# Performance work log

Hardware: AMD Instinct MI355X
Metric: run time of the kernel (lower is better)

## Reference

```python
import jax, jax.numpy as jnp
import numpy as np

B, N, M, D, H, K, V = 2, 2048, 2048, 1024, 16, 64, 64
MAX_WAVELENGTH = 10000
SCALE_FACTOR = 1.0


def rope(x, positions, max_wavelength, scale_factor):
    # x: [b, s, h, k]; positions: [b, s] int
    head_dim = x.shape[-1]
    fraction = 2.0 * jnp.arange(head_dim // 2, dtype=x.dtype) / head_dim
    timescale = jnp.asarray(max_wavelength, x.dtype) ** fraction            # [k/2]
    # scaled positions -> phase per (b, s, 1 head bcast, k/2)
    phase = (positions.astype(x.dtype) / scale_factor)[:, :, None, None] / timescale  # [b,s,1,k/2]
    sin, cos = jnp.sin(phase), jnp.cos(phase)
    x1, x2 = jnp.split(x, 2, axis=-1)
    return jnp.concatenate([x1 * cos - x2 * sin, x2 * cos + x1 * sin], axis=-1)


def setup_inputs() -> dict:
    key = jax.random.key(0)
    ks = jax.random.split(key, 8)
    scale = 1.0 / np.sqrt(D)  # keep logits numerically sane with random params
    inp = {
        "query": jax.random.normal(ks[0], (B, N, D), jnp.float32),
        "q_positions": jnp.broadcast_to(jnp.arange(N, dtype=jnp.int32), (B, N)),
        "key": jax.random.normal(ks[1], (B, M, D), jnp.float32),
        "k_positions": jnp.broadcast_to(jnp.arange(M, dtype=jnp.int32), (B, M)),
        "value": jax.random.normal(ks[2], (B, M, D), jnp.float32),
        "mask": jnp.ones((1, 1, N, M), dtype=bool),
        "P_q": jax.random.normal(ks[3], (H, D, K), jnp.float32) * scale,
        "P_k": jax.random.normal(ks[4], (H, D, K), jnp.float32) * scale,
        "P_v": jax.random.normal(ks[5], (H, D, V), jnp.float32) * scale,
        "P_o": jax.random.normal(ks[6], (H, D, V), jnp.float32) * scale,
    }
    return inp


def reference(query, q_positions, key, k_positions, value, mask, P_q, P_k, P_v, P_o):
    q = jnp.einsum('bnd,hdk->bnhk', query, P_q)
    k = jnp.einsum('bmd,hdk->bmhk', key, P_k)
    v = jnp.einsum('bmd,hdv->bmhv', value, P_v)
    q = rope(q, q_positions, MAX_WAVELENGTH, SCALE_FACTOR)
    k = rope(k, k_positions, MAX_WAVELENGTH, SCALE_FACTOR)
    logits = jnp.einsum('bnhk,bmhk->bhnm', q, k)
    if mask is not None:
        logits = jnp.where(mask, logits, -jnp.inf)
    weights = jax.nn.softmax(logits, axis=-1)
    o = jnp.einsum('bhnm,bmhv->bnhv', weights, v)
    return jnp.einsum('bnhv,hdv->bnd', o, P_o)
```

## Files before the change

kernel.cpp:

```cpp
#include <hip/hip_runtime.h>
#include <hip/hip_bf16.h>
#include <math.h>

#define B_ 2
#define N_ 2048
#define M_ 2048
#define D_ 1024
#define H_ 16


typedef _Float16 f16;
typedef f16  f16x4 __attribute__((ext_vector_type(4)));
typedef f16  f16x8 __attribute__((ext_vector_type(8)));
typedef float f32x4  __attribute__((ext_vector_type(4)));
typedef float f32x16 __attribute__((ext_vector_type(16)));

#define MFMA16(a, b, c) __builtin_amdgcn_mfma_f32_16x16x32_f16((a), (b), (c), 0, 0, 0)
#define MFMA32(a, b, c) __builtin_amdgcn_mfma_f32_32x32x16_f16((a), (b), (c), 0, 0, 0)
#define LDST 72

__global__ __launch_bounds__(256) void prep_pt(
    const float* __restrict__ P, f16* __restrict__ Pt)
{
  __shared__ float Ts[64][65];
  const int tid = threadIdx.x;
  const int d0 = blockIdx.x * 64, h = blockIdx.y;
  #pragma unroll
  for (int it = 0; it < 4; ++it) {
    int fi = tid + 256 * it;
    int dr = fi >> 4, c4 = (fi & 15) << 2;
    float4 v = *(const float4*)(P + ((size_t)h * D_ + d0 + dr) * 64 + c4);
    Ts[dr][c4+0] = v.x; Ts[dr][c4+1] = v.y; Ts[dr][c4+2] = v.z; Ts[dr][c4+3] = v.w;
  }
  __syncthreads();
  const int c = tid >> 2, dp = (tid & 3) * 16;
  f16x8 w0, w1;
  #pragma unroll
  for (int i = 0; i < 8; ++i) { w0[i] = (f16)Ts[dp + i][c]; w1[i] = (f16)Ts[dp + 8 + i][c]; }
  f16* dst = Pt + ((size_t)h * 64 + c) * D_ + d0 + dp;
  *(f16x8*)dst = w0;
  *(f16x8*)(dst + 8) = w1;
}

__global__ __launch_bounds__(256) void prep_wo(
    const float* __restrict__ Po, f16* __restrict__ Wo)
{
  int e = (blockIdx.x * 256 + threadIdx.x) * 4;
  if (e >= H_ * D_ * 64) return;
  int h = e >> 16, d = (e >> 6) & 1023, v = e & 63;
  float4 x = *(const float4*)(Po + e);
  f16x4 w = {(f16)x.x, (f16)x.y, (f16)x.z, (f16)x.w};
  *(f16x4*)&Wo[(size_t)d * 1024 + h * 64 + v] = w;
}

__global__ __launch_bounds__(256, 3) void gemm_fused(
    const float* __restrict__ Aq, const float* __restrict__ Ak,
    const float* __restrict__ Av,
    const f16* __restrict__ Bq, const f16* __restrict__ Bk,
    const f16* __restrict__ Bv,
    const int* __restrict__ qpos, const int* __restrict__ kpos,
    f16* __restrict__ dq, f16* __restrict__ dk, f16* __restrict__ dv)
{
  __shared__ f16 As[128 * LDST];
  __shared__ f16 Bs[128 * LDST];
  const int tid = threadIdx.x, lane = tid & 63, wave = tid >> 6;
  const int quad = lane >> 4, l16 = lane & 15;
  const int col0 = blockIdx.x * 128, row0 = blockIdx.y * 128;
  const int op = blockIdx.z;
  const int wr = (wave >> 1) * 64, wc = (wave & 1) * 64;

  const float* A  = (op == 0) ? Aq : (op == 1) ? Ak : Av;
  const f16*  Bt  = (op == 0) ? Bq : (op == 1) ? Bk : Bv;

  f32x4 acc[4][4] = {};

  for (int k0 = 0; k0 < 1024; k0 += 64) {
    #pragma unroll
    for (int it = 0; it < 8; ++it) {
      int fi = tid + 256 * it;
      int row = fi >> 4, c4 = (fi & 15) << 2;
      float4 xv = *(const float4*)(A + (size_t)(row0 + row) * 1024 + k0 + c4);
      f16x4 hv = {(f16)xv.x, (f16)xv.y, (f16)xv.z, (f16)xv.w};
      *(f16x4*)&As[row * LDST + c4] = hv;
    }
    #pragma unroll
    for (int it = 0; it < 4; ++it) {
      int fi = tid + 256 * it;
      int row = fi >> 3, c8 = (fi & 7) * 8;
      *(f16x8*)&Bs[row * LDST + c8] =
          *(const f16x8*)(Bt + (size_t)(col0 + row) * 1024 + k0 + c8);
    }
    __syncthreads();
    #pragma unroll
    for (int ks = 0; ks < 2; ++ks) {
      f16x8 af[4], bf[4];
      #pragma unroll
      for (int i = 0; i < 4; ++i)
        af[i] = *(const f16x8*)&As[(wr + i * 16 + l16) * LDST + ks * 32 + quad * 8];
      #pragma unroll
      for (int j = 0; j < 4; ++j)
        bf[j] = *(const f16x8*)&Bs[(wc + j * 16 + l16) * LDST + ks * 32 + quad * 8];
      #pragma unroll
      for (int i = 0; i < 4; ++i)
        #pragma unroll
        for (int j = 0; j < 4; ++j)
          acc[i][j] = MFMA16(af[i], bf[j], acc[i][j]);
    }
    __syncthreads();
  }

  if (op == 2) {
    #pragma unroll
    for (int i = 0; i < 4; ++i) {
      int r = row0 + wr + i * 16 + quad * 4;
      int b = r >> 11, s = r & 2047;
      #pragma unroll
      for (int j = 0; j < 4; ++j) {
        int col = col0 + wc + j * 16 + l16;
        int h = col >> 6, v = col & 63;
        f16x4 w = {(f16)acc[i][j][0], (f16)acc[i][j][1],
                   (f16)acc[i][j][2], (f16)acc[i][j][3]};
        *(f16x4*)&dv[((size_t)(b * H_ + h) * 64 + v) * 2048 + s] = w;
      }
    }
  } else {
    const int* pos = (op == 0) ? qpos : kpos;
    f16* oq = (op == 0) ? dq : dk;
    #pragma unroll
    for (int i = 0; i < 4; ++i) {
      #pragma unroll
      for (int reg = 0; reg < 4; ++reg) {
        int r = row0 + wr + i * 16 + quad * 4 + reg;
        int b = r >> 11, s = r & 2047;
        float fpos = (float)pos[r];
        #pragma unroll
        for (int j = 0; j < 2; ++j) {
          int col = col0 + wc + j * 16 + l16;
          int h = col >> 6, c = col & 63;
          float inv_ts = exp2f(-(float)c * 0.4152410118609203f);
          float ph = fpos * inv_ts, sn, cs;
          sincosf(ph, &sn, &cs);
          float x1 = acc[i][j][reg], x2 = acc[i][j + 2][reg];
          size_t base = ((size_t)(b * H_ + h) * 2048 + s) * 64;
          oq[base + c]      = (f16)(x1 * cs - x2 * sn);
          oq[base + c + 32] = (f16)(x2 * cs + x1 * sn);
        }
      }
    }
  }
}

__global__ __launch_bounds__(256) void flash4(
    const f16* __restrict__ q, const f16* __restrict__ k,
    const f16* __restrict__ vt, f16* __restrict__ o)
{
  __shared__ f16 Ks[64 * LDST];
  __shared__ f16 Vts[64 * LDST];
  __shared__ f16 Ps[4][32 * LDST];

  const int tid = threadIdx.x, lane = tid & 63, wave = tid >> 6;
  const int L = lane >> 5, nl = lane & 31;
  const int n0 = blockIdx.x * 128;
  const int h = blockIdx.y, b = blockIdx.z;

  const f16* qb = q  + (size_t)(b * H_ + h) * N_ * 64;
  const f16* kb = k  + (size_t)(b * H_ + h) * M_ * 64;
  const f16* vb = vt + (size_t)(b * H_ + h) * 64 * M_;

  f16x8 qf[4];
  #pragma unroll
  for (int g = 0; g < 4; ++g)
    qf[g] = *(const f16x8*)(qb + (size_t)(n0 + wave * 32 + nl) * 64 + g * 16 + L * 8);

  f32x16 acc[2] = {};
  float mst = -INFINITY;
  float lst = 0.f;
  const float L2E = 1.4426950408889634f;

  const int srow = tid >> 2, soff = (tid & 3) * 16;
  f16* psw = Ps[wave];

  for (int m0 = 0; m0 < M_; m0 += 64) {
    *(f16x8*)&Ks[srow * LDST + soff]      = *(const f16x8*)(kb + (size_t)(m0 + srow) * 64 + soff);
    *(f16x8*)&Ks[srow * LDST + soff + 8]  = *(const f16x8*)(kb + (size_t)(m0 + srow) * 64 + soff + 8);
    *(f16x8*)&Vts[srow * LDST + soff]     = *(const f16x8*)(vb + (size_t)srow * M_ + m0 + soff);
    *(f16x8*)&Vts[srow * LDST + soff + 8] = *(const f16x8*)(vb + (size_t)srow * M_ + m0 + soff + 8);
    __syncthreads();

    f32x16 s[2] = {};
    #pragma unroll
    for (int u = 0; u < 2; ++u)
      #pragma unroll
      for (int g = 0; g < 4; ++g) {
        f16x8 af = *(const f16x8*)&Ks[(u * 32 + nl) * LDST + g * 16 + L * 8];
        s[u] = MFMA32(af, qf[g], s[u]);
      }

    float mx = s[0][0];
    #pragma unroll
    for (int u = 0; u < 2; ++u)
      #pragma unroll
      for (int r = 0; r < 16; ++r) mx = fmaxf(mx, s[u][r]);
    mx = fmaxf(mx, __shfl_xor(mx, 32));
    float m_new = fmaxf(mst, mx * L2E);
    float alpha = exp2f(mst - m_new);
    mst = m_new;

    float sum = 0.f;
    float p[2][16];
    #pragma unroll
    for (int u = 0; u < 2; ++u)
      #pragma unroll
      for (int r = 0; r < 16; ++r) {
        float pv = exp2f(s[u][r] * L2E - m_new);
        p[u][r] = pv;
        sum += pv;
      }
    sum += __shfl_xor(sum, 32);
    lst = lst * alpha + sum;

    #pragma unroll
    for (int u = 0; u < 2; ++u)
      #pragma unroll
      for (int rq = 0; rq < 4; ++rq) {
        f16x4 w = {(f16)p[u][rq * 4 + 0], (f16)p[u][rq * 4 + 1],
                   (f16)p[u][rq * 4 + 2], (f16)p[u][rq * 4 + 3]};
        *(f16x4*)&psw[nl * LDST + u * 32 + 8 * rq + 4 * L] = w;
      }
    f16x8 pb[4];
    #pragma unroll
    for (int g = 0; g < 4; ++g)
      pb[g] = *(const f16x8*)&psw[nl * LDST + g * 16 + L * 8];

    #pragma unroll
    for (int u = 0; u < 2; ++u)
      #pragma unroll
      for (int r = 0; r < 16; ++r) acc[u][r] *= alpha;
    #pragma unroll
    for (int u = 0; u < 2; ++u)
      #pragma unroll
      for (int g = 0; g < 4; ++g) {
        f16x8 vf = *(const f16x8*)&Vts[(u * 32 + nl) * LDST + g * 16 + L * 8];
        acc[u] = MFMA32(vf, pb[g], acc[u]);
      }
    __syncthreads();
  }

  float invl = 1.0f / lst;
  f16* ob = o + ((size_t)(b * N_ + n0 + wave * 32 + nl) * 1024) + h * 64;
  #pragma unroll
  for (int u = 0; u < 2; ++u)
    #pragma unroll
    for (int rq = 0; rq < 4; ++rq) {
      f16x4 w = {(f16)(acc[u][rq * 4 + 0] * invl), (f16)(acc[u][rq * 4 + 1] * invl),
                 (f16)(acc[u][rq * 4 + 2] * invl), (f16)(acc[u][rq * 4 + 3] * invl)};
      *(f16x4*)&ob[u * 32 + 8 * rq + 4 * L] = w;
    }
}

__global__ __launch_bounds__(256) void gemm_out(
    const f16* __restrict__ A, const f16* __restrict__ Bt,
    float* __restrict__ out)
{
  __shared__ f16 As[128 * LDST];
  __shared__ f16 Bs[64 * LDST];
  const int tid = threadIdx.x, lane = tid & 63, wave = tid >> 6;
  const int quad = lane >> 4, l16 = lane & 15;
  const int col0 = blockIdx.x * 64, row0 = blockIdx.y * 128;
  const int wr = (wave >> 1) * 64, wc = (wave & 1) * 32;

  f32x4 acc[4][2] = {};

  for (int k0 = 0; k0 < 1024; k0 += 64) {
    #pragma unroll
    for (int it = 0; it < 4; ++it) {
      int fi = tid + 256 * it;
      int row = fi >> 3, c8 = (fi & 7) * 8;
      *(f16x8*)&As[row * LDST + c8] =
          *(const f16x8*)(A + (size_t)(row0 + row) * 1024 + k0 + c8);
    }
    #pragma unroll
    for (int it = 0; it < 2; ++it) {
      int fi = tid + 256 * it;
      int row = fi >> 3, c8 = (fi & 7) * 8;
      *(f16x8*)&Bs[row * LDST + c8] =
          *(const f16x8*)(Bt + (size_t)(col0 + row) * 1024 + k0 + c8);
    }
    __syncthreads();
    #pragma unroll
    for (int ks = 0; ks < 2; ++ks) {
      f16x8 af[4], bf[2];
      #pragma unroll
      for (int i = 0; i < 4; ++i)
        af[i] = *(const f16x8*)&As[(wr + i * 16 + l16) * LDST + ks * 32 + quad * 8];
      #pragma unroll
      for (int j = 0; j < 2; ++j)
        bf[j] = *(const f16x8*)&Bs[(wc + j * 16 + l16) * LDST + ks * 32 + quad * 8];
      #pragma unroll
      for (int i = 0; i < 4; ++i)
        #pragma unroll
        for (int j = 0; j < 2; ++j)
          acc[i][j] = MFMA16(af[i], bf[j], acc[i][j]);
    }
    __syncthreads();
  }

  #pragma unroll
  for (int i = 0; i < 4; ++i)
    #pragma unroll
    for (int j = 0; j < 2; ++j)
      #pragma unroll
      for (int reg = 0; reg < 4; ++reg)
        out[(size_t)(row0 + wr + i * 16 + quad * 4 + reg) * 1024 +
            col0 + wc + j * 16 + l16] = acc[i][j][reg];
}

extern "C" void kernel_launch(void* const* d_in, const int* in_sizes, int n_in,
                              void* d_out, int out_size, void* d_ws, size_t ws_size,
                              hipStream_t stream) {
  (void)in_sizes; (void)n_in; (void)out_size; (void)ws_size;
  const float* query = (const float*)d_in[0];
  const int*   qpos  = (const int*)d_in[1];
  const float* key   = (const float*)d_in[2];
  const int*   kpos  = (const int*)d_in[3];
  const float* value = (const float*)d_in[4];
  const float* Pq = (const float*)d_in[6];
  const float* Pk = (const float*)d_in[7];
  const float* Pv = (const float*)d_in[8];
  const float* Po = (const float*)d_in[9];
  float* out = (float*)d_out;

  const size_t pm = (size_t)1024 * 1024;
  const size_t em = (size_t)B_ * H_ * 2048 * 64;
  f16* Ptq = (f16*)d_ws;
  f16* Ptk = Ptq + pm;
  f16* Ptv = Ptk + pm;
  f16* Wo  = Ptv + pm;
  f16* q_ws  = Wo + pm;
  f16* k_ws  = q_ws + em;
  f16* vt_ws = k_ws + em;
  f16* o_ws  = vt_ws + em;

  dim3 blk(256);
  prep_pt<<<dim3(16, 16), blk, 0, stream>>>(Pq, Ptq);
  prep_pt<<<dim3(16, 16), blk, 0, stream>>>(Pk, Ptk);
  prep_pt<<<dim3(16, 16), blk, 0, stream>>>(Pv, Ptv);
  prep_wo<<<dim3(1024), blk, 0, stream>>>(Po, Wo);

  gemm_fused<<<dim3(8, 32, 3), blk, 0, stream>>>(
      query, key, value, Ptq, Ptk, Ptv, qpos, kpos, q_ws, k_ws, vt_ws);

  flash4<<<dim3(N_ / 128, H_, B_), blk, 0, stream>>>(q_ws, k_ws, vt_ws, o_ws);

  gemm_out<<<dim3(16, 32), blk, 0, stream>>>(o_ws, Wo, out);
}
```

Baseline: 280.0 us.

## Prefetch tiles into registers, merge prep kernels, precompute RoPE tables, skip rescale

```diff
diff --git a/kernel.cpp b/kernel.cpp
--- a/kernel.cpp
+++ b/kernel.cpp
@@ -19,46 +19,62 @@
 #define MFMA32(a, b, c) __builtin_amdgcn_mfma_f32_32x32x16_f16((a), (b), (c), 0, 0, 0)
 #define LDST 72
 
-__global__ __launch_bounds__(256) void prep_pt(
-    const float* __restrict__ P, f16* __restrict__ Pt)
+__global__ __launch_bounds__(256) void prep_all(
+    const float* __restrict__ Pq, const float* __restrict__ Pk,
+    const float* __restrict__ Pv, const float* __restrict__ Po,
+    const int* __restrict__ qpos, const int* __restrict__ kpos,
+    f16* __restrict__ Ptq, f16* __restrict__ Ptk, f16* __restrict__ Ptv,
+    f16* __restrict__ Wo, float2* __restrict__ tabq, float2* __restrict__ tabk)
 {
   __shared__ float Ts[64][65];
-  const int tid = threadIdx.x;
-  const int d0 = blockIdx.x * 64, h = blockIdx.y;
-  #pragma unroll
-  for (int it = 0; it < 4; ++it) {
-    int fi = tid + 256 * it;
-    int dr = fi >> 4, c4 = (fi & 15) << 2;
-    float4 v = *(const float4*)(P + ((size_t)h * D_ + d0 + dr) * 64 + c4);
-    Ts[dr][c4+0] = v.x; Ts[dr][c4+1] = v.y; Ts[dr][c4+2] = v.z; Ts[dr][c4+3] = v.w;
-  }
-  __syncthreads();
-  const int c = tid >> 2, dp = (tid & 3) * 16;
-  f16x8 w0, w1;
-  #pragma unroll
-  for (int i = 0; i < 8; ++i) { w0[i] = (f16)Ts[dp + i][c]; w1[i] = (f16)Ts[dp + 8 + i][c]; }
-  f16* dst = Pt + ((size_t)h * 64 + c) * D_ + d0 + dp;
-  *(f16x8*)dst = w0;
-  *(f16x8*)(dst + 8) = w1;
+  const int z = blockIdx.y, x = blockIdx.x, tid = threadIdx.x;
+  if (z < 3) {
+    if (x >= 256) return;
+    const float* P = (z == 0) ? Pq : (z == 1) ? Pk : Pv;
+    f16* Pt = (z == 0) ? Ptq : (z == 1) ? Ptk : Ptv;
+    const int d0 = (x & 15) * 64, h = x >> 4;
+    #pragma unroll
+    for (int it = 0; it < 4; ++it) {
+      int fi = tid + 256 * it;
+      int dr = fi >> 4, c4 = (fi & 15) << 2;
+      float4 v = *(const float4*)(P + ((size_t)h * D_ + d0 + dr) * 64 + c4);
+      Ts[dr][c4+0] = v.x; Ts[dr][c4+1] = v.y; Ts[dr][c4+2] = v.z; Ts[dr][c4+3] = v.w;
+    }
+    __syncthreads();
+    const int c = tid >> 2, dp = (tid & 3) * 16;
+    f16x8 w0, w1;
+    #pragma unroll
+    for (int i = 0; i < 8; ++i) { w0[i] = (f16)Ts[dp + i][c]; w1[i] = (f16)Ts[dp + 8 + i][c]; }
+    f16* dst = Pt + ((size_t)h * 64 + c) * D_ + d0 + dp;
+    *(f16x8*)dst = w0;
+    *(f16x8*)(dst + 8) = w1;
+  } else if (z == 3) {
+    int e = (x * 256 + tid) * 4;
+    if (e >= H_ * D_ * 64) return;
+    int h = e >> 16, d = (e >> 6) & 1023, v = e & 63;
+    float4 xx = *(const float4*)(Po + e);
+    f16x4 w = {(f16)xx.x, (f16)xx.y, (f16)xx.z, (f16)xx.w};
+    *(f16x4*)&Wo[(size_t)d * 1024 + h * 64 + v] = w;
+  } else {
+    if (x >= 512) return;
+    int idx = x * 256 + tid;
+    int r = idx >> 5, c = idx & 31;
+    const int* pos = (z == 4) ? qpos : kpos;
+    float2* tab = (z == 4) ? tabq : tabk;
+    float fpos = (float)pos[r];
+    float inv_ts = exp2f(-(float)c * 0.4152410118609203f);
+    float ph = fpos * inv_ts, sn, cs;
+    sincosf(ph, &sn, &cs);
+    tab[idx] = make_float2(cs, sn);
+  }
 }
 
-__global__ __launch_bounds__(256) void prep_wo(
-    const float* __restrict__ Po, f16* __restrict__ Wo)
-{
-  int e = (blockIdx.x * 256 + threadIdx.x) * 4;
-  if (e >= H_ * D_ * 64) return;
-  int h = e >> 16, d = (e >> 6) & 1023, v = e & 63;
-  float4 x = *(const float4*)(Po + e);
-  f16x4 w = {(f16)x.x, (f16)x.y, (f16)x.z, (f16)x.w};
-  *(f16x4*)&Wo[(size_t)d * 1024 + h * 64 + v] = w;
-}
-
-__global__ __launch_bounds__(256, 3) void gemm_fused(
+__global__ __launch_bounds__(256) void gemm_fused(
     const float* __restrict__ Aq, const float* __restrict__ Ak,
     const float* __restrict__ Av,
     const f16* __restrict__ Bq, const f16* __restrict__ Bk,
     const f16* __restrict__ Bv,
-    const int* __restrict__ qpos, const int* __restrict__ kpos,
+    const float2* __restrict__ tabq, const float2* __restrict__ tabk,
     f16* __restrict__ dq, f16* __restrict__ dk, f16* __restrict__ dv)
 {
   __shared__ f16 As[128 * LDST];
@@ -73,24 +89,52 @@
   const f16*  Bt  = (op == 0) ? Bq : (op == 1) ? Bk : Bv;
 
   f32x4 acc[4][4] = {};
+  float4 apre[8];
+  f16x8  bpre[4];
+
+  #pragma unroll
+  for (int it = 0; it < 8; ++it) {
+    int fi = tid + 256 * it;
+    int row = fi >> 4, c4 = (fi & 15) << 2;
+    apre[it] = *(const float4*)(A + (size_t)(row0 + row) * 1024 + c4);
+  }
+  #pragma unroll
+  for (int it = 0; it < 4; ++it) {
+    int fi = tid + 256 * it;
+    int row = fi >> 3, c8 = (fi & 7) * 8;
+    bpre[it] = *(const f16x8*)(Bt + (size_t)(col0 + row) * 1024 + c8);
+  }
 
   for (int k0 = 0; k0 < 1024; k0 += 64) {
+    __syncthreads();
     #pragma unroll
     for (int it = 0; it < 8; ++it) {
       int fi = tid + 256 * it;
       int row = fi >> 4, c4 = (fi & 15) << 2;
-      float4 xv = *(const float4*)(A + (size_t)(row0 + row) * 1024 + k0 + c4);
-      f16x4 hv = {(f16)xv.x, (f16)xv.y, (f16)xv.z, (f16)xv.w};
+      f16x4 hv = {(f16)apre[it].x, (f16)apre[it].y, (f16)apre[it].z, (f16)apre[it].w};
       *(f16x4*)&As[row * LDST + c4] = hv;
     }
     #pragma unroll
     for (int it = 0; it < 4; ++it) {
       int fi = tid + 256 * it;
       int row = fi >> 3, c8 = (fi & 7) * 8;
-      *(f16x8*)&Bs[row * LDST + c8] =
-          *(const f16x8*)(Bt + (size_t)(col0 + row) * 1024 + k0 + c8);
-    }
-    __syncthreads();
+      *(f16x8*)&Bs[row * LDST + c8] = bpre[it];
+    }
+    __syncthreads();
+    if (k0 + 64 < 1024) {
+      #pragma unroll
+      for (int it = 0; it < 8; ++it) {
+        int fi = tid + 256 * it;
+        int row = fi >> 4, c4 = (fi & 15) << 2;
+        apre[it] = *(const float4*)(A + (size_t)(row0 + row) * 1024 + k0 + 64 + c4);
+      }
+      #pragma unroll
+      for (int it = 0; it < 4; ++it) {
+        int fi = tid + 256 * it;
+        int row = fi >> 3, c8 = (fi & 7) * 8;
+        bpre[it] = *(const f16x8*)(Bt + (size_t)(col0 + row) * 1024 + k0 + 64 + c8);
+      }
+    }
     #pragma unroll
     for (int ks = 0; ks < 2; ++ks) {
       f16x8 af[4], bf[4];
@@ -106,7 +150,6 @@
         for (int j = 0; j < 4; ++j)
           acc[i][j] = MFMA16(af[i], bf[j], acc[i][j]);
     }
-    __syncthreads();
   }
 
   if (op == 2) {
@@ -124,7 +167,7 @@
       }
     }
   } else {
-    const int* pos = (op == 0) ? qpos : kpos;
+    const float2* tab = (op == 0) ? tabq : tabk;
     f16* oq = (op == 0) ? dq : dk;
     #pragma unroll
     for (int i = 0; i < 4; ++i) {
@@ -132,25 +175,22 @@
       for (int reg = 0; reg < 4; ++reg) {
         int r = row0 + wr + i * 16 + quad * 4 + reg;
         int b = r >> 11, s = r & 2047;
-        float fpos = (float)pos[r];
         #pragma unroll
         for (int j = 0; j < 2; ++j) {
           int col = col0 + wc + j * 16 + l16;
           int h = col >> 6, c = col & 63;
-          float inv_ts = exp2f(-(float)c * 0.4152410118609203f);
-          float ph = fpos * inv_ts, sn, cs;
-          sincosf(ph, &sn, &cs);
+          float2 cs = tab[r * 32 + c];
           float x1 = acc[i][j][reg], x2 = acc[i][j + 2][reg];
           size_t base = ((size_t)(b * H_ + h) * 2048 + s) * 64;
-          oq[base + c]      = (f16)(x1 * cs - x2 * sn);
-          oq[base + c + 32] = (f16)(x2 * cs + x1 * sn);
+          oq[base + c]      = (f16)(x1 * cs.x - x2 * cs.y);
+          oq[base + c + 32] = (f16)(x2 * cs.x + x1 * cs.y);
         }
       }
     }
   }
 }
 
-__global__ __launch_bounds__(256) void flash4(
+__global__ __launch_bounds__(256) void flash5(
     const f16* __restrict__ q, const f16* __restrict__ k,
     const f16* __restrict__ vt, f16* __restrict__ o)
 {
@@ -180,12 +220,24 @@
   const int srow = tid >> 2, soff = (tid & 3) * 16;
   f16* psw = Ps[wave];
 
+  f16x8 kp0 = *(const f16x8*)(kb + (size_t)srow * 64 + soff);
+  f16x8 kp1 = *(const f16x8*)(kb + (size_t)srow * 64 + soff + 8);
+  f16x8 vp0 = *(const f16x8*)(vb + (size_t)srow * M_ + soff);
+  f16x8 vp1 = *(const f16x8*)(vb + (size_t)srow * M_ + soff + 8);
+
   for (int m0 = 0; m0 < M_; m0 += 64) {
-    *(f16x8*)&Ks[srow * LDST + soff]      = *(const f16x8*)(kb + (size_t)(m0 + srow) * 64 + soff);
-    *(f16x8*)&Ks[srow * LDST + soff + 8]  = *(const f16x8*)(kb + (size_t)(m0 + srow) * 64 + soff + 8);
-    *(f16x8*)&Vts[srow * LDST + soff]     = *(const f16x8*)(vb + (size_t)srow * M_ + m0 + soff);
-    *(f16x8*)&Vts[srow * LDST + soff + 8] = *(const f16x8*)(vb + (size_t)srow * M_ + m0 + soff + 8);
-    __syncthreads();
+    __syncthreads();
+    *(f16x8*)&Ks[srow * LDST + soff]      = kp0;
+    *(f16x8*)&Ks[srow * LDST + soff + 8]  = kp1;
+    *(f16x8*)&Vts[srow * LDST + soff]     = vp0;
+    *(f16x8*)&Vts[srow * LDST + soff + 8] = vp1;
+    __syncthreads();
+    if (m0 + 64 < M_) {
+      kp0 = *(const f16x8*)(kb + (size_t)(m0 + 64 + srow) * 64 + soff);
+      kp1 = *(const f16x8*)(kb + (size_t)(m0 + 64 + srow) * 64 + soff + 8);
+      vp0 = *(const f16x8*)(vb + (size_t)srow * M_ + m0 + 64 + soff);
+      vp1 = *(const f16x8*)(vb + (size_t)srow * M_ + m0 + 64 + soff + 8);
+    }
 
     f32x16 s[2] = {};
     #pragma unroll
@@ -203,7 +255,15 @@
       for (int r = 0; r < 16; ++r) mx = fmaxf(mx, s[u][r]);
     mx = fmaxf(mx, __shfl_xor(mx, 32));
     float m_new = fmaxf(mst, mx * L2E);
-    float alpha = exp2f(mst - m_new);
+    bool chg = (m_new > mst);
+    if (__ballot(chg)) {
+      float alpha = exp2f(mst - m_new);
+      #pragma unroll
+      for (int u = 0; u < 2; ++u)
+        #pragma unroll
+        for (int r = 0; r < 16; ++r) acc[u][r] *= alpha;
+      lst *= alpha;
+    }
     mst = m_new;
 
     float sum = 0.f;
@@ -217,7 +277,7 @@
         sum += pv;
       }
     sum += __shfl_xor(sum, 32);
-    lst = lst * alpha + sum;
+    lst += sum;
 
     #pragma unroll
     for (int u = 0; u < 2; ++u)
@@ -235,15 +295,10 @@
     #pragma unroll
     for (int u = 0; u < 2; ++u)
       #pragma unroll
-      for (int r = 0; r < 16; ++r) acc[u][r] *= alpha;
-    #pragma unroll
-    for (int u = 0; u < 2; ++u)
-      #pragma unroll
       for (int g = 0; g < 4; ++g) {
         f16x8 vf = *(const f16x8*)&Vts[(u * 32 + nl) * LDST + g * 16 + L * 8];
         acc[u] = MFMA32(vf, pb[g], acc[u]);
       }
-    __syncthreads();
   }
 
   float invl = 1.0f / lst;
@@ -270,23 +325,50 @@
   const int wr = (wave >> 1) * 64, wc = (wave & 1) * 32;
 
   f32x4 acc[4][2] = {};
+  f16x8 apre[4], bpre[2];
+
+  #pragma unroll
+  for (int it = 0; it < 4; ++it) {
+    int fi = tid + 256 * it;
+    int row = fi >> 3, c8 = (fi & 7) * 8;
+    apre[it] = *(const f16x8*)(A + (size_t)(row0 + row) * 1024 + c8);
+  }
+  #pragma unroll
+  for (int it = 0; it < 2; ++it) {
+    int fi = tid + 256 * it;
+    int row = fi >> 3, c8 = (fi & 7) * 8;
+    bpre[it] = *(const f16x8*)(Bt + (size_t)(col0 + row) * 1024 + c8);
+  }
 
   for (int k0 = 0; k0 < 1024; k0 += 64) {
+    __syncthreads();
     #pragma unroll
     for (int it = 0; it < 4; ++it) {
       int fi = tid + 256 * it;
       int row = fi >> 3, c8 = (fi & 7) * 8;
-      *(f16x8*)&As[row * LDST + c8] =
-          *(const f16x8*)(A + (size_t)(row0 + row) * 1024 + k0 + c8);
+      *(f16x8*)&As[row * LDST + c8] = apre[it];
     }
     #pragma unroll
     for (int it = 0; it < 2; ++it) {
       int fi = tid + 256 * it;
       int row = fi >> 3, c8 = (fi & 7) * 8;
-      *(f16x8*)&Bs[row * LDST + c8] =
-          *(const f16x8*)(Bt + (size_t)(col0 + row) * 1024 + k0 + c8);
-    }
-    __syncthreads();
+      *(f16x8*)&Bs[row * LDST + c8] = bpre[it];
+    }
+    __syncthreads();
+    if (k0 + 64 < 1024) {
+      #pragma unroll
+      for (int it = 0; it < 4; ++it) {
+        int fi = tid + 256 * it;
+        int row = fi >> 3, c8 = (fi & 7) * 8;
+        apre[it] = *(const f16x8*)(A + (size_t)(row0 + row) * 1024 + k0 + 64 + c8);
+      }
+      #pragma unroll
+      for (int it = 0; it < 2; ++it) {
+        int fi = tid + 256 * it;
+        int row = fi >> 3, c8 = (fi & 7) * 8;
+        bpre[it] = *(const f16x8*)(Bt + (size_t)(col0 + row) * 1024 + k0 + 64 + c8);
+      }
+    }
     #pragma unroll
     for (int ks = 0; ks < 2; ++ks) {
       f16x8 af[4], bf[2];
@@ -302,7 +384,6 @@
         for (int j = 0; j < 2; ++j)
           acc[i][j] = MFMA16(af[i], bf[j], acc[i][j]);
     }
-    __syncthreads();
   }
 
   #pragma unroll
@@ -340,17 +421,17 @@
   f16* k_ws  = q_ws + em;
   f16* vt_ws = k_ws + em;
   f16* o_ws  = vt_ws + em;
+  float2* tabq = (float2*)(o_ws + em);
+  float2* tabk = tabq + (size_t)4096 * 32;
 
   dim3 blk(256);
-  prep_pt<<<dim3(16, 16), blk, 0, stream>>>(Pq, Ptq);
-  prep_pt<<<dim3(16, 16), blk, 0, stream>>>(Pk, Ptk);
-  prep_pt<<<dim3(16, 16), blk, 0, stream>>>(Pv, Ptv);
-  prep_wo<<<dim3(1024), blk, 0, stream>>>(Po, Wo);
+  prep_all<<<dim3(1024, 6), blk, 0, stream>>>(
+      Pq, Pk, Pv, Po, qpos, kpos, Ptq, Ptk, Ptv, Wo, tabq, tabk);
 
   gemm_fused<<<dim3(8, 32, 3), blk, 0, stream>>>(
-      query, key, value, Ptq, Ptk, Ptv, qpos, kpos, q_ws, k_ws, vt_ws);
-
-  flash4<<<dim3(N_ / 128, H_, B_), blk, 0, stream>>>(q_ws, k_ws, vt_ws, o_ws);
+      query, key, value, Ptq, Ptk, Ptv, tabq, tabk, q_ws, k_ws, vt_ws);
+
+  flash5<<<dim3(N_ / 128, H_, B_), blk, 0, stream>>>(q_ws, k_ws, vt_ws, o_ws);
 
   gemm_out<<<dim3(16, 32), blk, 0, stream>>>(o_ws, Wo, out);
 }
```

Result: faster. 271.9 us (-2.9%).
